# Kernel tuning notes

Measured on AMD Instinct MI355X. Metric: run time of the kernel, lower is better.

Reference implementation:

```python
import jax, jax.numpy as jnp
import numpy as np
from jax import lax

HEADS, DIM_HEAD, KSZ = 8, 64, 3


def conv1x1(x, w):
    # x: [B, Cin, X, Y], w: [Cout, Cin]
    return jnp.einsum('oi,bixy->boxy', w, x)


def setup_inputs() -> dict:
    key = jax.random.key(0)
    ks = jax.random.split(key, 8)
    dim = 256
    inner = HEADS * DIM_HEAD  # 512
    B, H, W = 4, 64, 64
    s = 0.02
    return {
        'fmap': jax.random.normal(ks[0], (B, dim, H, W), jnp.float32),
        'w_lin_q': jax.random.normal(ks[1], (inner, dim), jnp.float32) * s,
        'w_lin_kv_dw': jax.random.normal(ks[2], (dim, 1, 3, 3), jnp.float32) * s,
        'w_lin_kv_pw': jax.random.normal(ks[3], (2 * inner, dim), jnp.float32) * s,
        'w_q': jax.random.normal(ks[4], (inner, dim), jnp.float32) * s,
        'w_kv': jax.random.normal(ks[5], (2 * inner, dim), jnp.float32) * s,
        'w_out': jax.random.normal(ks[6], (dim, 2 * inner), jnp.float32) * s,
        'b_out': jax.random.normal(ks[7], (dim,), jnp.float32) * s,
    }


def reference(fmap, w_lin_q, w_lin_kv_dw, w_lin_kv_pw, w_q, w_kv, w_out, b_out):
    B, dim, X, Y = fmap.shape
    h, d, ksz = HEADS, DIM_HEAD, KSZ
    scale = d ** -0.5
    n = X * Y

    # ---- linear (global) attention branch ----
    # depthwise 3x3 conv (groups=dim) then pointwise 1x1, both bias-free
    dw = lax.conv_general_dilated(
        fmap, w_lin_kv_dw, window_strides=(1, 1), padding=[(1, 1), (1, 1)],
        dimension_numbers=('NCHW', 'OIHW', 'NCHW'), feature_group_count=dim)
    lin_kv = conv1x1(dw, w_lin_kv_pw)
    lin_q = conv1x1(fmap, w_lin_q)
    lin_k, lin_v = jnp.split(lin_kv, 2, axis=1)

    def to_bhnd(t):  # [B, h*d, X, Y] -> [B, h, n, d]
        return t.reshape(B, h, d, n).transpose(0, 1, 3, 2)

    lq, lk, lv = to_bhnd(lin_q), to_bhnd(lin_k), to_bhnd(lin_v)
    lq = jax.nn.softmax(lq, axis=-1) * scale   # softmax over feature dim
    lk = jax.nn.softmax(lk, axis=-2)           # softmax over sequence dim
    ctx = jnp.einsum('bhnd,bhne->bhde', lk, lv)
    lin_out = jnp.einsum('bhnd,bhde->bhne', lq, ctx)
    lin_out = lin_out.transpose(0, 1, 3, 2).reshape(B, h * d, X, Y)
    lin_out = jax.nn.gelu(lin_out, approximate=False)  # torch nn.GELU (exact erf)

    # ---- local window attention branch (unfold equivalent) ----
    q = conv1x1(fmap, w_q).reshape(B, h, d, X, Y) * scale
    kv = conv1x1(fmap, w_kv)
    k, v = jnp.split(kv, 2, axis=1)
    k = k.reshape(B, h, d, X, Y)
    v = v.reshape(B, h, d, X, Y)
    pad = ksz // 2
    padw = ((0, 0), (0, 0), (0, 0), (pad, pad), (pad, pad))
    kp = jnp.pad(k, padw)  # zero padding, as in F.unfold
    vp = jnp.pad(v, padw)
    # j enumerates kernel offsets row-major (ky, kx) -> matches F.unfold layout
    k_win = jnp.stack([kp[..., i:i + X, j:j + Y]
                       for i in range(ksz) for j in range(ksz)], axis=2)  # [B,h,j,d,X,Y]
    v_win = jnp.stack([vp[..., i:i + X, j:j + Y]
                       for i in range(ksz) for j in range(ksz)], axis=2)
    sim = jnp.einsum('bhdxy,bhjdxy->bhxyj', q, k_win)
    attn = jax.nn.softmax(sim, axis=-1)  # stable (max-subtracted internally)
    full = jnp.einsum('bhxyj,bhjdxy->bhdxy', attn, v_win)
    full = full.reshape(B, h * d, X, Y)

    out = jnp.concatenate([lin_out, full], axis=1)  # [B, 2*inner, X, Y]
    return conv1x1(out, w_out) + b_out[None, :, None, None]
```

## Files before the change

kernel.cpp:

```cpp
#include <hip/hip_runtime.h>
#include <cmath>

#define NPIX 4096
#define NTOT 16384
#define CIN  256

typedef __bf16 bf16x8 __attribute__((ext_vector_type(8)));
typedef float  f32x4  __attribute__((ext_vector_type(4)));
typedef unsigned short u16x8 __attribute__((ext_vector_type(8)));

static __device__ __forceinline__ unsigned short f2bf(float f) {
    unsigned u = __float_as_uint(f);
    unsigned r = (u + 0x7FFFu + ((u >> 16) & 1u)) >> 16;
    return (unsigned short)r;
}
static __device__ __forceinline__ float bf2f(unsigned short u) {
    return __uint_as_float((unsigned)u << 16);
}

__global__ __launch_bounds__(256) void k_transpose_bf(const float* __restrict__ src,
                                                      unsigned short* __restrict__ dst) {
    __shared__ float tile[64][65];
    int p0 = blockIdx.x * 64;
    int c0 = blockIdx.y * 64;
    int b  = blockIdx.z;
    int t = threadIdx.x;
    int tp = t & 63, tg = t >> 6;
    const float* s = src + ((size_t)(b * 256 + c0) * 4096) + p0;
#pragma unroll
    for (int r = 0; r < 16; ++r) {
        int c = r * 4 + tg;
        tile[tp][c] = s[(size_t)c * 4096 + tp];
    }
    __syncthreads();
    unsigned short* d = dst + ((size_t)(b * 4096 + p0)) * 256 + c0;
#pragma unroll
    for (int r = 0; r < 16; ++r) {
        int pr = r * 4 + tg;
        d[(size_t)pr * 256 + tp] = f2bf(tile[pr][tp]);
    }
}

__global__ __launch_bounds__(256) void k_dwconv_bf(const unsigned short* __restrict__ FMB,
                                                   const float* __restrict__ wdw,
                                                   unsigned short* __restrict__ DWB) {
    __shared__ float wl[2560];
    int t = threadIdx.x;
    for (int i = t; i < 2304; i += 256) wl[(i / 9) * 10 + (i % 9)] = wdw[i];
    __syncthreads();
    int idx = blockIdx.x * 256 + t;
    int cg = idx & 31, p = idx >> 5;
    int xy = p & 4095, x = xy >> 6, y = xy & 63;
    const unsigned short* base = FMB + (size_t)p * 256 + cg * 8;
    float s[8] = {0.f, 0.f, 0.f, 0.f, 0.f, 0.f, 0.f, 0.f};
#pragma unroll
    for (int dx = 0; dx < 3; ++dx) {
        int xx = x + dx - 1;
        if ((unsigned)xx >= 64u) continue;
#pragma unroll
        for (int dy = 0; dy < 3; ++dy) {
            int yy = y + dy - 1;
            if ((unsigned)yy >= 64u) continue;
            u16x8 v = *(const u16x8*)(base + ((dx - 1) * 64 + (dy - 1)) * 256);
#pragma unroll
            for (int d = 0; d < 8; ++d)
                s[d] += bf2f(v[d]) * wl[(cg * 8 + d) * 10 + dx * 3 + dy];
        }
    }
    uint4 w0;
    w0.x = (unsigned)f2bf(s[0]) | ((unsigned)f2bf(s[1]) << 16);
    w0.y = (unsigned)f2bf(s[2]) | ((unsigned)f2bf(s[3]) << 16);
    w0.z = (unsigned)f2bf(s[4]) | ((unsigned)f2bf(s[5]) << 16);
    w0.w = (unsigned)f2bf(s[6]) | ((unsigned)f2bf(s[7]) << 16);
    *(uint4*)(DWB + (size_t)p * 256 + cg * 8) = w0;
}

__global__ __launch_bounds__(256) void k_convert_w(const float* __restrict__ w1, const float* __restrict__ w2,
                                                   const float* __restrict__ w3, const float* __restrict__ w4,
                                                   const float* __restrict__ w5,
                                                   unsigned short* __restrict__ dst) {
    int i = blockIdx.x * 256 + threadIdx.x;
    float v;
    if (i < 131072)       v = w1[i];
    else if (i < 262144)  v = w2[i - 131072];
    else if (i < 524288)  v = w3[i - 262144];
    else if (i < 786432) {
        int elem = i - 524288;
        int rp = elem >> 8, c = elem & 255;
        int h = rp >> 7, wi = rp & 127;
        int srow = (wi < 64) ? (h * 64 + wi) : (512 + h * 64 + (wi - 64));
        v = w4[srow * 256 + c];
    } else                v = w5[i - 786432];
    dst[i] = f2bf(v);
}

__global__ __launch_bounds__(256) void k_qkv_gemm(const __bf16* __restrict__ FMB,
                                                  const __bf16* __restrict__ DWB,
                                                  const __bf16* __restrict__ WQKV,
                                                  const __bf16* __restrict__ WPW,
                                                  unsigned short* __restrict__ LQB,
                                                  unsigned short* __restrict__ CKV2,
                                                  float* __restrict__ PART,
                                                  float* __restrict__ S) {
    __shared__ __align__(16) __bf16 SMEM[128 * 136];
    __bf16* As = SMEM;
    __bf16* Bs = SMEM + 128 * 64;
    const int K = 256;
    const int m0 = blockIdx.x * 128;
    const int by = blockIdx.y;
    const bool g2 = (by >= 16);
    const __bf16* A = g2 ? DWB : FMB;
    const __bf16* B = g2 ? WPW : WQKV;
    const int n0 = (g2 ? by - 16 : by) * 128;
    const int t = threadIdx.x;
    const int w = t >> 6, l = t & 63;
    const int wm = (w >> 1) * 64, wn = (w & 1) * 64;
    f32x4 acc[4][4];
#pragma unroll
    for (int i = 0; i < 4; ++i)
#pragma unroll
        for (int j = 0; j < 4; ++j) acc[i][j] = (f32x4){0.f, 0.f, 0.f, 0.f};

    const int lrow = l >> 3;
    const int lchunk = (l & 7) ^ lrow;
    for (int k0 = 0; k0 < K; k0 += 64) {
#pragma unroll
        for (int r = 0; r < 4; ++r) {
            const int s = w + r * 4;
            const int row = s * 8 + lrow;
            const __bf16* ga = A + (size_t)(m0 + row) * K + (k0 + lchunk * 8);
            const __bf16* gb = B + (size_t)(n0 + row) * K + (k0 + lchunk * 8);
            __builtin_amdgcn_global_load_lds((const __attribute__((address_space(1))) void*)ga,
                                             (__attribute__((address_space(3))) void*)(As + s * 512),
                                             16, 0, 0);
            __builtin_amdgcn_global_load_lds((const __attribute__((address_space(1))) void*)gb,
                                             (__attribute__((address_space(3))) void*)(Bs + s * 512),
                                             16, 0, 0);
        }
        __syncthreads();
#pragma unroll
        for (int ks = 0; ks < 2; ++ks) {
            bf16x8 af[4], bfr[4];
#pragma unroll
            for (int i = 0; i < 4; ++i) {
                const int arow = wm + i * 16 + (l & 15);
                const int ac = ((l >> 4) + ks * 4) ^ (l & 7);
                af[i] = *(const bf16x8*)(As + arow * 64 + ac * 8);
                const int brow = wn + i * 16 + (l & 15);
                bfr[i] = *(const bf16x8*)(Bs + brow * 64 + ac * 8);
            }
#pragma unroll
            for (int i = 0; i < 4; ++i)
#pragma unroll
                for (int j = 0; j < 4; ++j)
                    acc[i][j] = __builtin_amdgcn_mfma_f32_16x16x32_bf16(af[i], bfr[j], acc[i][j], 0, 0, 0);
        }
        __syncthreads();
    }

    if (g2) {
        unsigned short* ST = (unsigned short*)SMEM;
#pragma unroll
        for (int i = 0; i < 4; ++i) {
            const int prow = wm + i * 16 + (l >> 4) * 4;
#pragma unroll
            for (int j = 0; j < 4; ++j) {
                const int col = wn + j * 16 + (l & 15);
#pragma unroll
                for (int q = 0; q < 4; ++q) {
                    float v = acc[i][j][q];
                    ST[col * 130 + prow + q] = f2bf(col < 64 ? __expf(v) : v);
                }
            }
        }
        __syncthreads();
        const int h  = n0 >> 7;
        const int bh = (m0 >> 12) * 8 + h;
        const int dm = (w >> 1) * 32, en = (w & 1) * 32;
        f32x4 c2[2][2];
        f32x4 s2[2];
#pragma unroll
        for (int i = 0; i < 2; ++i) {
            s2[i] = (f32x4){0.f, 0.f, 0.f, 0.f};
#pragma unroll
            for (int j = 0; j < 2; ++j) c2[i][j] = (f32x4){0.f, 0.f, 0.f, 0.f};
        }
        bf16x8 ones;
#pragma unroll
        for (int d = 0; d < 8; ++d) ones[d] = (__bf16)1.0f;
#pragma unroll
        for (int kp = 0; kp < 4; ++kp) {
            bf16x8 af2[2], bv2[2];
#pragma unroll
            for (int i = 0; i < 2; ++i) {
                const int drow = dm + i * 16 + (l & 15);
                af2[i] = *(const bf16x8*)(ST + drow * 130 + kp * 32 + (l >> 4) * 8);
                const int erow = 64 + en + i * 16 + (l & 15);
                bv2[i] = *(const bf16x8*)(ST + erow * 130 + kp * 32 + (l >> 4) * 8);
            }
#pragma unroll
            for (int i = 0; i < 2; ++i)
#pragma unroll
                for (int j = 0; j < 2; ++j)
                    c2[i][j] = __builtin_amdgcn_mfma_f32_16x16x32_bf16(af2[i], bv2[j], c2[i][j], 0, 0, 0);
            if ((w & 1) == 0)
#pragma unroll
                for (int i = 0; i < 2; ++i)
                    s2[i] = __builtin_amdgcn_mfma_f32_16x16x32_bf16(af2[i], ones, s2[i], 0, 0, 0);
        }
        float* pp = PART + ((size_t)((m0 >> 7) * 8 + h)) * 4096 + t * 16;
#pragma unroll
        for (int i = 0; i < 2; ++i)
#pragma unroll
            for (int j = 0; j < 2; ++j)
                *(f32x4*)(pp + (i * 2 + j) * 4) = c2[i][j];
        if ((w & 1) == 0 && (l & 15) == 0) {
#pragma unroll
            for (int i = 0; i < 2; ++i)
#pragma unroll
                for (int q = 0; q < 4; ++q)
                    atomicAdd(&S[bh * 64 + dm + i * 16 + (l >> 4) * 4 + q], s2[i][q]);
        }
        return;
    }

#pragma unroll
    for (int i = 0; i < 4; ++i) {
        const int prow = wm + i * 16 + (l >> 4) * 4;
#pragma unroll
        for (int j = 0; j < 4; ++j) {
            const int col = wn + j * 16 + (l & 15);
            const int cglob = n0 + col;
            const float sc = (cglob >= 512 && cglob < 1024) ? 0.125f : 1.f;
#pragma unroll
            for (int q = 0; q < 4; ++q)
                *((unsigned short*)SMEM + (prow + q) * 136 + col) = f2bf(acc[i][j][q] * sc);
        }
    }
    __syncthreads();
    const int pix = t >> 1, half = t & 1;
    const unsigned short* sp = (const unsigned short*)SMEM + pix * 136 + half * 64;
    if (n0 < 512) {
        float m = -1e30f;
#pragma unroll
        for (int r = 0; r < 8; ++r) {
            u16x8 v = *(const u16x8*)(sp + r * 8);
#pragma unroll
            for (int d = 0; d < 8; ++d) m = fmaxf(m, bf2f(v[d]));
        }
        float Z = 0.f;
#pragma unroll
        for (int r = 0; r < 8; ++r) {
            u16x8 v = *(const u16x8*)(sp + r * 8);
#pragma unroll
            for (int d = 0; d < 8; ++d) Z += __expf(bf2f(v[d]) - m);
        }
        float inv = 0.125f / Z;
        unsigned short* dst = LQB + (size_t)(m0 + pix) * 512 + n0 + half * 64;
#pragma unroll
        for (int r = 0; r < 8; ++r) {
            u16x8 v = *(const u16x8*)(sp + r * 8);
            float o[8];
#pragma unroll
            for (int d = 0; d < 8; ++d) o[d] = __expf(bf2f(v[d]) - m) * inv;
            uint4 wv;
            wv.x = (unsigned)f2bf(o[0]) | ((unsigned)f2bf(o[1]) << 16);
            wv.y = (unsigned)f2bf(o[2]) | ((unsigned)f2bf(o[3]) << 16);
            wv.z = (unsigned)f2bf(o[4]) | ((unsigned)f2bf(o[5]) << 16);
            wv.w = (unsigned)f2bf(o[6]) | ((unsigned)f2bf(o[7]) << 16);
            *(uint4*)(dst + r * 8) = wv;
        }
    } else {
        unsigned short* dptr = CKV2 + (size_t)(m0 + pix) * 1536 + (n0 - 512) + half * 64;
#pragma unroll
        for (int r = 0; r < 8; ++r)
            *(u16x8*)(dptr + r * 8) = *(const u16x8*)(sp + r * 8);
    }
}

__global__ __launch_bounds__(256) void k_ctxnorm(const float* __restrict__ PART,
                                                 const float* __restrict__ S,
                                                 unsigned short* __restrict__ ctxb) {
    __shared__ float SUM[1024];
    __shared__ float sinv[32];
    const int bh = blockIdx.x, wq = blockIdx.y;
    const int b = bh >> 3, h = bh & 7;
    const int t = threadIdx.x;
    const int bd = (wq >> 1) * 32, be = (wq & 1) * 32;
#pragma unroll
    for (int r = 0; r < 4; ++r) {
        const int kl = t + 256 * r;
        const float* src = PART + (size_t)((b * 32) * 8 + h) * 4096 + wq * 1024 + kl;
        float s = 0.f;
#pragma unroll
        for (int mi = 0; mi < 32; ++mi)
            s += src[(size_t)mi * 8 * 4096];
        SUM[kl] = s;
    }
    if (t < 32) sinv[t] = 1.f / S[bh * 64 + bd + t];
    __syncthreads();
#pragma unroll
    for (int r = 0; r < 4; ++r) {
        const int idx = t + 256 * r;
        const int dd = idx & 31, ee = idx >> 5;
        const int d = bd + dd, e = be + ee;
        const int l2 = (((d >> 2) & 3) << 4) | (e & 15);
        const int i2 = (d >> 4) & 1, j2 = (e >> 4) & 1, q = d & 3;
        const int kl = l2 * 16 + (i2 * 2 + j2) * 4 + q;
        ctxb[(size_t)bh * 4096 + e * 64 + d] = f2bf(SUM[kl] * sinv[dd]);
    }
}

__global__ __launch_bounds__(256) void k_out_gemm(const __bf16* __restrict__ A,
                                                  const __bf16* __restrict__ B,
                                                  float* __restrict__ C,
                                                  const float* __restrict__ bias) {
    __shared__ __align__(16) __bf16 SMEM[24576];
    const int K = 1024;
    const int m0 = blockIdx.x * 64, n0 = blockIdx.y * 128;
    const int t = threadIdx.x;
    const int w = t >> 6, l = t & 63;
    const int wm = (w >> 1) * 32, wn = (w & 1) * 64;
    f32x4 acc[2][4];
#pragma unroll
    for (int i = 0; i < 2; ++i)
#pragma unroll
        for (int j = 0; j < 4; ++j) acc[i][j] = (f32x4){0.f, 0.f, 0.f, 0.f};

    const int lrow = l >> 3;
    const int lchunk = (l & 7) ^ lrow;
    auto stage = [&](int buf, int k0) {
        __bf16* As = SMEM + buf * 12288;
        __bf16* Bs = As + 4096;
#pragma unroll
        for (int r = 0; r < 2; ++r) {
            const int s = w + r * 4;
            const int row = s * 8 + lrow;
            const __bf16* ga = A + (size_t)(m0 + row) * K + (k0 + lchunk * 8);
            __builtin_amdgcn_global_load_lds((const __attribute__((address_space(1))) void*)ga,
                                             (__attribute__((address_space(3))) void*)(As + s * 512),
                                             16, 0, 0);
        }
#pragma unroll
        for (int r = 0; r < 4; ++r) {
            const int s = w + r * 4;
            const int row = s * 8 + lrow;
            const __bf16* gb = B + (size_t)(n0 + row) * K + (k0 + lchunk * 8);
            __builtin_amdgcn_global_load_lds((const __attribute__((address_space(1))) void*)gb,
                                             (__attribute__((address_space(3))) void*)(Bs + s * 512),
                                             16, 0, 0);
        }
    };

    stage(0, 0);
    for (int it = 0; it < 16; ++it) {
        __syncthreads();
        if (it < 15) stage((it + 1) & 1, (it + 1) * 64);
        const __bf16* As = SMEM + (it & 1) * 12288;
        const __bf16* Bs = As + 4096;
#pragma unroll
        for (int ks = 0; ks < 2; ++ks) {
            const int ac = ((l >> 4) + ks * 4) ^ (l & 7);
            bf16x8 af[2], bfr[4];
#pragma unroll
            for (int i = 0; i < 2; ++i) {
                const int arow = wm + i * 16 + (l & 15);
                af[i] = *(const bf16x8*)(As + arow * 64 + ac * 8);
            }
#pragma unroll
            for (int j = 0; j < 4; ++j) {
                const int brow = wn + j * 16 + (l & 15);
                bfr[j] = *(const bf16x8*)(Bs + brow * 64 + ac * 8);
            }
#pragma unroll
            for (int i = 0; i < 2; ++i)
#pragma unroll
                for (int j = 0; j < 4; ++j)
                    acc[i][j] = __builtin_amdgcn_mfma_f32_16x16x32_bf16(af[i], bfr[j], acc[i][j], 0, 0, 0);
        }
    }
    const int b = m0 >> 12;
#pragma unroll
    for (int j = 0; j < 4; ++j) {
        const int col = n0 + wn + j * 16 + (l & 15);
        const float bv = bias[col];
        float* obase = C + ((size_t)(b * 256 + col) << 12);
#pragma unroll
        for (int i = 0; i < 2; ++i) {
            const int rb = (m0 & 4095) + wm + i * 16 + (l >> 4) * 4;
            f32x4 v = acc[i][j];
            v[0] += bv; v[1] += bv; v[2] += bv; v[3] += bv;
            *(f32x4*)(obase + rb) = v;
        }
    }
}

__global__ __launch_bounds__(256) void k_lin_mfma(const __bf16* __restrict__ LQB,
                                                  const __bf16* __restrict__ ctxb,
                                                  unsigned short* __restrict__ CAT) {
    const int p0 = blockIdx.x * 128;
    const int h  = blockIdx.y;
    const int b  = p0 >> 12;
    const int t = threadIdx.x, w = t >> 6, l = t & 63;
    const int wm = w * 32;
    const __bf16* Bm = ctxb + (size_t)(b * 8 + h) * 4096;
    f32x4 acc[2][4];
#pragma unroll
    for (int i = 0; i < 2; ++i)
#pragma unroll
        for (int j = 0; j < 4; ++j) acc[i][j] = (f32x4){0.f, 0.f, 0.f, 0.f};
#pragma unroll
    for (int ks = 0; ks < 2; ++ks) {
        const int c = (l >> 4) + ks * 4;
        bf16x8 af[2], bfr[4];
#pragma unroll
        for (int i = 0; i < 2; ++i) {
            const int row = p0 + wm + i * 16 + (l & 15);
            af[i] = *(const bf16x8*)(LQB + (size_t)row * 512 + h * 64 + c * 8);
        }
#pragma unroll
        for (int j = 0; j < 4; ++j) {
            const int erow = j * 16 + (l & 15);
            bfr[j] = *(const bf16x8*)(Bm + erow * 64 + c * 8);
        }
#pragma unroll
        for (int i = 0; i < 2; ++i)
#pragma unroll
            for (int j = 0; j < 4; ++j)
                acc[i][j] = __builtin_amdgcn_mfma_f32_16x16x32_bf16(af[i], bfr[j], acc[i][j], 0, 0, 0);
    }
#pragma unroll
    for (int i = 0; i < 2; ++i) {
#pragma unroll
        for (int j = 0; j < 4; ++j) {
            const int e = j * 16 + (l & 15);
#pragma unroll
            for (int q = 0; q < 4; ++q) {
                const int p = p0 + wm + i * 16 + (l >> 4) * 4 + q;
                float x = acc[i][j][q];
                float g = 0.5f * x * (1.f + erff(x * 0.70710678118654752f));
                CAT[(size_t)p * 1024 + h * 64 + e] = f2bf(g);
            }
        }
    }
}

__global__ __launch_bounds__(256) void k_local_attn(const unsigned short* __restrict__ CKV,
                                                    unsigned short* __restrict__ CAT) {
    const int W = blockIdx.x * 4 + (threadIdx.x >> 6);
    const int lane = threadIdx.x & 63;
    const int h = W & 7;
    const int G = W >> 3;
    const int yg = G & 7, x = (G >> 3) & 63, b = G >> 9;
    const int lg = lane >> 3, c8 = lane & 7;
    const int y = (yg << 3) + lg;
    const int p = (b << 12) + (x << 6) + y;
    const unsigned short* Qp = CKV + (size_t)p * 1536 + h * 64 + c8 * 8;
    const unsigned short* Kp = Qp + 512;
    const unsigned short* Vp = Qp + 1024;

    const bool okx[3] = {x > 0, true, x < 63};
    const bool oky[3] = {y > 0, true, y < 63};
    bool okn[9]; int ofs[9];
#pragma unroll
    for (int dx = 0; dx < 3; ++dx)
#pragma unroll
        for (int dy = 0; dy < 3; ++dy) {
            const int k = dx * 3 + dy;
            okn[k] = okx[dx] && oky[dy];
            ofs[k] = okn[k] ? ((dx - 1) * 64 + (dy - 1)) * 1536 : 0;
        }
    float qf[8];
    {
        u16x8 q8 = *(const u16x8*)Qp;
#pragma unroll
        for (int d = 0; d < 8; ++d) qf[d] = bf2f(q8[d]);
    }
    float sim[9];
#pragma unroll
    for (int k = 0; k < 9; ++k) {
        u16x8 k8 = *(const u16x8*)(Kp + ofs[k]);
        float s = 0.f;
#pragma unroll
        for (int d = 0; d < 8; ++d) s += qf[d] * bf2f(k8[d]);
        s = okn[k] ? s : 0.f;
        s += __shfl_xor(s, 1);
        s += __shfl_xor(s, 2);
        s += __shfl_xor(s, 4);
        sim[k] = s;
    }
    float mx = sim[0];
#pragma unroll
    for (int k = 1; k < 9; ++k) mx = fmaxf(mx, sim[k]);
    float a[9], Z = 0.f;
#pragma unroll
    for (int k = 0; k < 9; ++k) { a[k] = __expf(sim[k] - mx); Z += a[k]; }
    float inv = 1.f / Z;
#pragma unroll
    for (int k = 0; k < 9; ++k) a[k] = okn[k] ? a[k] * inv : 0.f;
    float o[8] = {0.f, 0.f, 0.f, 0.f, 0.f, 0.f, 0.f, 0.f};
#pragma unroll
    for (int k = 0; k < 9; ++k) {
        u16x8 v8 = *(const u16x8*)(Vp + ofs[k]);
#pragma unroll
        for (int d = 0; d < 8; ++d) o[d] += a[k] * bf2f(v8[d]);
    }
    unsigned short* dst = CAT + (size_t)p * 1024 + 512 + h * 64 + c8 * 8;
    uint4 w0;
    w0.x = (unsigned)f2bf(o[0]) | ((unsigned)f2bf(o[1]) << 16);
    w0.y = (unsigned)f2bf(o[2]) | ((unsigned)f2bf(o[3]) << 16);
    w0.z = (unsigned)f2bf(o[4]) | ((unsigned)f2bf(o[5]) << 16);
    w0.w = (unsigned)f2bf(o[6]) | ((unsigned)f2bf(o[7]) << 16);
    *(uint4*)dst = w0;
}

extern "C" void kernel_launch(void* const* d_in, const int* in_sizes, int n_in,
                              void* d_out, int out_size, void* d_ws, size_t ws_size,
                              hipStream_t stream) {
    const float* fmap  = (const float*)d_in[0];
    const float* w_lq  = (const float*)d_in[1];
    const float* w_dw  = (const float*)d_in[2];
    const float* w_pw  = (const float*)d_in[3];
    const float* w_q   = (const float*)d_in[4];
    const float* w_kv  = (const float*)d_in[5];
    const float* w_out = (const float*)d_in[6];
    const float* b_out = (const float*)d_in[7];
    float* out = (float*)d_out;

    unsigned short* base = (unsigned short*)d_ws;
    unsigned short* CATB = base;
    unsigned short* FMB  = base + (size_t)NTOT * 1024;
    unsigned short* DWB  = FMB + (size_t)NTOT * 256;
    unsigned short* WB   = DWB + (size_t)NTOT * 256;
    unsigned short* WQKV = WB;
    unsigned short* WPW  = WB + 524288;
    unsigned short* WOUT = WB + 786432;
    unsigned short* CTXB = WB + 1048576;
    unsigned short* LQB  = CTXB + 131072;
    unsigned short* CKV2 = LQB + (size_t)NTOT * 512;
    float* PART = (float*)(CKV2 + (size_t)NTOT * 1536);
    float* S    = PART + (size_t)1024 * 4096;

    k_transpose_bf<<<dim3(64, 4, 4), 256, 0, stream>>>(fmap, FMB);
    k_convert_w<<<4096, 256, 0, stream>>>(w_lq, w_q, w_kv, w_pw, w_out, WB);
    hipMemsetAsync(S, 0, 2048 * sizeof(float), stream);
    k_dwconv_bf<<<2048, 256, 0, stream>>>(FMB, w_dw, DWB);
    k_qkv_gemm<<<dim3(128, 24), 256, 0, stream>>>((const __bf16*)FMB, (const __bf16*)DWB,
                                                  (const __bf16*)WQKV, (const __bf16*)WPW,
                                                  LQB, CKV2, PART, S);
    k_ctxnorm<<<dim3(32, 4), 256, 0, stream>>>(PART, S, CTXB);
    k_lin_mfma<<<dim3(128, 8), 256, 0, stream>>>((const __bf16*)LQB, (const __bf16*)CTXB, CATB);
    k_local_attn<<<4096, 256, 0, stream>>>(CKV2, CATB);
    k_out_gemm<<<dim3(256, 2), 256, 0, stream>>>((const __bf16*)CATB, (const __bf16*)WOUT, out, b_out);
}
```

Before: 166.0 us.

## Double-buffer GEMM loads with prefetch depth two and merge lin/local attention kernels

The QKV GEMM now double-buffers its LDS tiles and issues the next two k-stages ahead, using explicit vmcnt waits and raw barriers in place of __syncthreads. The output GEMM likewise prefetches two stages ahead with partial vmcnt waits. The linear-attention MFMA kernel and the local window attention kernel are fused into one launch that branches on block index, which removes a launch and lets both workloads share the GPU. This adds more LDS per block in the QKV GEMM, which may lower occupancy, and relies on hand-counted vmcnt values being correct.

```diff
diff --git a/kernel.cpp b/kernel.cpp
--- a/kernel.cpp
+++ b/kernel.cpp
@@ -102,9 +102,7 @@
                                                   unsigned short* __restrict__ CKV2,
                                                   float* __restrict__ PART,
                                                   float* __restrict__ S) {
-    __shared__ __align__(16) __bf16 SMEM[128 * 136];
-    __bf16* As = SMEM;
-    __bf16* Bs = SMEM + 128 * 64;
+    __shared__ __align__(16) __bf16 SMEM[32768];
     const int K = 256;
     const int m0 = blockIdx.x * 128;
     const int by = blockIdx.y;
@@ -123,7 +121,7 @@
 
     const int lrow = l >> 3;
     const int lchunk = (l & 7) ^ lrow;
-    for (int k0 = 0; k0 < K; k0 += 64) {
+    auto STAGE = [&](int buf, int k0) {
 #pragma unroll
         for (int r = 0; r < 4; ++r) {
             const int s = w + r * 4;
@@ -131,13 +129,24 @@
             const __bf16* ga = A + (size_t)(m0 + row) * K + (k0 + lchunk * 8);
             const __bf16* gb = B + (size_t)(n0 + row) * K + (k0 + lchunk * 8);
             __builtin_amdgcn_global_load_lds((const __attribute__((address_space(1))) void*)ga,
-                                             (__attribute__((address_space(3))) void*)(As + s * 512),
+                                             (__attribute__((address_space(3))) void*)(SMEM + buf * 16384 + s * 512),
                                              16, 0, 0);
             __builtin_amdgcn_global_load_lds((const __attribute__((address_space(1))) void*)gb,
-                                             (__attribute__((address_space(3))) void*)(Bs + s * 512),
+                                             (__attribute__((address_space(3))) void*)(SMEM + buf * 16384 + 8192 + s * 512),
                                              16, 0, 0);
         }
-        __syncthreads();
+    };
+    STAGE(0, 0);
+    STAGE(1, 64);
+#pragma unroll
+    for (int it = 0; it < 4; ++it) {
+        if (it < 3) { asm volatile("s_waitcnt vmcnt(8)" ::: "memory"); }
+        else        { asm volatile("s_waitcnt vmcnt(0)" ::: "memory"); }
+        __builtin_amdgcn_sched_barrier(0);
+        __builtin_amdgcn_s_barrier();
+        __builtin_amdgcn_sched_barrier(0);
+        const __bf16* As = SMEM + (it & 1) * 16384;
+        const __bf16* Bs = As + 8192;
 #pragma unroll
         for (int ks = 0; ks < 2; ++ks) {
             bf16x8 af[4], bfr[4];
@@ -155,7 +164,10 @@
                 for (int j = 0; j < 4; ++j)
                     acc[i][j] = __builtin_amdgcn_mfma_f32_16x16x32_bf16(af[i], bfr[j], acc[i][j], 0, 0, 0);
         }
-        __syncthreads();
+        __builtin_amdgcn_sched_barrier(0);
+        __builtin_amdgcn_s_barrier();
+        __builtin_amdgcn_sched_barrier(0);
+        if (it < 2) STAGE(it & 1, (it + 2) * 64);
     }
 
     if (g2) {
@@ -329,7 +341,7 @@
 
     const int lrow = l >> 3;
     const int lchunk = (l & 7) ^ lrow;
-    auto stage = [&](int buf, int k0) {
+    auto STAGE = [&](int buf, int k0) {
         __bf16* As = SMEM + buf * 12288;
         __bf16* Bs = As + 4096;
 #pragma unroll
@@ -352,10 +364,14 @@
         }
     };
 
-    stage(0, 0);
+    STAGE(0, 0);
+    STAGE(1, 64);
     for (int it = 0; it < 16; ++it) {
-        __syncthreads();
-        if (it < 15) stage((it + 1) & 1, (it + 1) * 64);
+        if (it < 15) { asm volatile("s_waitcnt vmcnt(6)" ::: "memory"); }
+        else         { asm volatile("s_waitcnt vmcnt(0)" ::: "memory"); }
+        __builtin_amdgcn_sched_barrier(0);
+        __builtin_amdgcn_s_barrier();
+        __builtin_amdgcn_sched_barrier(0);
         const __bf16* As = SMEM + (it & 1) * 12288;
         const __bf16* Bs = As + 4096;
 #pragma unroll
@@ -378,6 +394,10 @@
                 for (int j = 0; j < 4; ++j)
                     acc[i][j] = __builtin_amdgcn_mfma_f32_16x16x32_bf16(af[i], bfr[j], acc[i][j], 0, 0, 0);
         }
+        __builtin_amdgcn_sched_barrier(0);
+        __builtin_amdgcn_s_barrier();
+        __builtin_amdgcn_sched_barrier(0);
+        if (it < 14) STAGE(it & 1, (it + 2) * 64);
     }
     const int b = m0 >> 12;
 #pragma unroll
@@ -395,123 +415,125 @@
     }
 }
 
-__global__ __launch_bounds__(256) void k_lin_mfma(const __bf16* __restrict__ LQB,
+__global__ __launch_bounds__(256) void k_linlocal(const __bf16* __restrict__ LQB,
                                                   const __bf16* __restrict__ ctxb,
+                                                  const unsigned short* __restrict__ CKV,
                                                   unsigned short* __restrict__ CAT) {
-    const int p0 = blockIdx.x * 128;
-    const int h  = blockIdx.y;
-    const int b  = p0 >> 12;
-    const int t = threadIdx.x, w = t >> 6, l = t & 63;
-    const int wm = w * 32;
-    const __bf16* Bm = ctxb + (size_t)(b * 8 + h) * 4096;
-    f32x4 acc[2][4];
-#pragma unroll
-    for (int i = 0; i < 2; ++i)
-#pragma unroll
-        for (int j = 0; j < 4; ++j) acc[i][j] = (f32x4){0.f, 0.f, 0.f, 0.f};
-#pragma unroll
-    for (int ks = 0; ks < 2; ++ks) {
-        const int c = (l >> 4) + ks * 4;
-        bf16x8 af[2], bfr[4];
+    const int bid = blockIdx.x;
+    const int t = threadIdx.x;
+    if (bid < 1024) {
+        const int p0 = (bid & 127) * 128;
+        const int h  = bid >> 7;
+        const int b  = p0 >> 12;
+        const int w = t >> 6, l = t & 63;
+        const int wm = w * 32;
+        const __bf16* Bm = ctxb + (size_t)(b * 8 + h) * 4096;
+        f32x4 acc[2][4];
+#pragma unroll
+        for (int i = 0; i < 2; ++i)
+#pragma unroll
+            for (int j = 0; j < 4; ++j) acc[i][j] = (f32x4){0.f, 0.f, 0.f, 0.f};
+#pragma unroll
+        for (int ks = 0; ks < 2; ++ks) {
+            const int c = (l >> 4) + ks * 4;
+            bf16x8 af[2], bfr[4];
+#pragma unroll
+            for (int i = 0; i < 2; ++i) {
+                const int row = p0 + wm + i * 16 + (l & 15);
+                af[i] = *(const bf16x8*)(LQB + (size_t)row * 512 + h * 64 + c * 8);
+            }
+#pragma unroll
+            for (int j = 0; j < 4; ++j) {
+                const int erow = j * 16 + (l & 15);
+                bfr[j] = *(const bf16x8*)(Bm + erow * 64 + c * 8);
+            }
+#pragma unroll
+            for (int i = 0; i < 2; ++i)
+#pragma unroll
+                for (int j = 0; j < 4; ++j)
+                    acc[i][j] = __builtin_amdgcn_mfma_f32_16x16x32_bf16(af[i], bfr[j], acc[i][j], 0, 0, 0);
+        }
 #pragma unroll
         for (int i = 0; i < 2; ++i) {
-            const int row = p0 + wm + i * 16 + (l & 15);
-            af[i] = *(const bf16x8*)(LQB + (size_t)row * 512 + h * 64 + c * 8);
-        }
-#pragma unroll
-        for (int j = 0; j < 4; ++j) {
-            const int erow = j * 16 + (l & 15);
-            bfr[j] = *(const bf16x8*)(Bm + erow * 64 + c * 8);
-        }
-#pragma unroll
-        for (int i = 0; i < 2; ++i)
-#pragma unroll
-            for (int j = 0; j < 4; ++j)
-                acc[i][j] = __builtin_amdgcn_mfma_f32_16x16x32_bf16(af[i], bfr[j], acc[i][j], 0, 0, 0);
-    }
-#pragma unroll
-    for (int i = 0; i < 2; ++i) {
-#pragma unroll
-        for (int j = 0; j < 4; ++j) {
-            const int e = j * 16 + (l & 15);
-#pragma unroll
-            for (int q = 0; q < 4; ++q) {
-                const int p = p0 + wm + i * 16 + (l >> 4) * 4 + q;
-                float x = acc[i][j][q];
-                float g = 0.5f * x * (1.f + erff(x * 0.70710678118654752f));
-                CAT[(size_t)p * 1024 + h * 64 + e] = f2bf(g);
-            }
-        }
-    }
-}
-
-__global__ __launch_bounds__(256) void k_local_attn(const unsigned short* __restrict__ CKV,
-                                                    unsigned short* __restrict__ CAT) {
-    const int W = blockIdx.x * 4 + (threadIdx.x >> 6);
-    const int lane = threadIdx.x & 63;
-    const int h = W & 7;
-    const int G = W >> 3;
-    const int yg = G & 7, x = (G >> 3) & 63, b = G >> 9;
-    const int lg = lane >> 3, c8 = lane & 7;
-    const int y = (yg << 3) + lg;
-    const int p = (b << 12) + (x << 6) + y;
-    const unsigned short* Qp = CKV + (size_t)p * 1536 + h * 64 + c8 * 8;
-    const unsigned short* Kp = Qp + 512;
-    const unsigned short* Vp = Qp + 1024;
-
-    const bool okx[3] = {x > 0, true, x < 63};
-    const bool oky[3] = {y > 0, true, y < 63};
-    bool okn[9]; int ofs[9];
-#pragma unroll
-    for (int dx = 0; dx < 3; ++dx)
-#pragma unroll
-        for (int dy = 0; dy < 3; ++dy) {
-            const int k = dx * 3 + dy;
-            okn[k] = okx[dx] && oky[dy];
-            ofs[k] = okn[k] ? ((dx - 1) * 64 + (dy - 1)) * 1536 : 0;
-        }
-    float qf[8];
-    {
-        u16x8 q8 = *(const u16x8*)Qp;
-#pragma unroll
-        for (int d = 0; d < 8; ++d) qf[d] = bf2f(q8[d]);
-    }
-    float sim[9];
-#pragma unroll
-    for (int k = 0; k < 9; ++k) {
-        u16x8 k8 = *(const u16x8*)(Kp + ofs[k]);
-        float s = 0.f;
-#pragma unroll
-        for (int d = 0; d < 8; ++d) s += qf[d] * bf2f(k8[d]);
-        s = okn[k] ? s : 0.f;
-        s += __shfl_xor(s, 1);
-        s += __shfl_xor(s, 2);
-        s += __shfl_xor(s, 4);
-        sim[k] = s;
-    }
-    float mx = sim[0];
-#pragma unroll
-    for (int k = 1; k < 9; ++k) mx = fmaxf(mx, sim[k]);
-    float a[9], Z = 0.f;
-#pragma unroll
-    for (int k = 0; k < 9; ++k) { a[k] = __expf(sim[k] - mx); Z += a[k]; }
-    float inv = 1.f / Z;
-#pragma unroll
-    for (int k = 0; k < 9; ++k) a[k] = okn[k] ? a[k] * inv : 0.f;
-    float o[8] = {0.f, 0.f, 0.f, 0.f, 0.f, 0.f, 0.f, 0.f};
-#pragma unroll
-    for (int k = 0; k < 9; ++k) {
-        u16x8 v8 = *(const u16x8*)(Vp + ofs[k]);
-#pragma unroll
-        for (int d = 0; d < 8; ++d) o[d] += a[k] * bf2f(v8[d]);
-    }
-    unsigned short* dst = CAT + (size_t)p * 1024 + 512 + h * 64 + c8 * 8;
-    uint4 w0;
-    w0.x = (unsigned)f2bf(o[0]) | ((unsigned)f2bf(o[1]) << 16);
-    w0.y = (unsigned)f2bf(o[2]) | ((unsigned)f2bf(o[3]) << 16);
-    w0.z = (unsigned)f2bf(o[4]) | ((unsigned)f2bf(o[5]) << 16);
-    w0.w = (unsigned)f2bf(o[6]) | ((unsigned)f2bf(o[7]) << 16);
-    *(uint4*)dst = w0;
+#pragma unroll
+            for (int j = 0; j < 4; ++j) {
+                const int e = j * 16 + (l & 15);
+#pragma unroll
+                for (int q = 0; q < 4; ++q) {
+                    const int p = p0 + wm + i * 16 + (l >> 4) * 4 + q;
+                    float x = acc[i][j][q];
+                    float g = 0.5f * x * (1.f + erff(x * 0.70710678118654752f));
+                    CAT[(size_t)p * 1024 + h * 64 + e] = f2bf(g);
+                }
+            }
+        }
+    } else {
+        const int W = (bid - 1024) * 4 + (t >> 6);
+        const int lane = t & 63;
+        const int h = W & 7;
+        const int G = W >> 3;
+        const int yg = G & 7, x = (G >> 3) & 63, b = G >> 9;
+        const int lg = lane >> 3, c8 = lane & 7;
+        const int y = (yg << 3) + lg;
+        const int p = (b << 12) + (x << 6) + y;
+        const unsigned short* Qp = CKV + (size_t)p * 1536 + h * 64 + c8 * 8;
+        const unsigned short* Kp = Qp + 512;
+        const unsigned short* Vp = Qp + 1024;
+
+        const bool okx[3] = {x > 0, true, x < 63};
+        const bool oky[3] = {y > 0, true, y < 63};
+        bool okn[9]; int ofs[9];
+#pragma unroll
+        for (int dx = 0; dx < 3; ++dx)
+#pragma unroll
+            for (int dy = 0; dy < 3; ++dy) {
+                const int k = dx * 3 + dy;
+                okn[k] = okx[dx] && oky[dy];
+                ofs[k] = okn[k] ? ((dx - 1) * 64 + (dy - 1)) * 1536 : 0;
+            }
+        float qf[8];
+        {
+            u16x8 q8 = *(const u16x8*)Qp;
+#pragma unroll
+            for (int d = 0; d < 8; ++d) qf[d] = bf2f(q8[d]);
+        }
+        float sim[9];
+#pragma unroll
+        for (int k = 0; k < 9; ++k) {
+            u16x8 k8 = *(const u16x8*)(Kp + ofs[k]);
+            float s = 0.f;
+#pragma unroll
+            for (int d = 0; d < 8; ++d) s += qf[d] * bf2f(k8[d]);
+            s = okn[k] ? s : 0.f;
+            s += __shfl_xor(s, 1);
+            s += __shfl_xor(s, 2);
+            s += __shfl_xor(s, 4);
+            sim[k] = s;
+        }
+        float mx = sim[0];
+#pragma unroll
+        for (int k = 1; k < 9; ++k) mx = fmaxf(mx, sim[k]);
+        float a[9], Z = 0.f;
+#pragma unroll
+        for (int k = 0; k < 9; ++k) { a[k] = __expf(sim[k] - mx); Z += a[k]; }
+        float inv = 1.f / Z;
+#pragma unroll
+        for (int k = 0; k < 9; ++k) a[k] = okn[k] ? a[k] * inv : 0.f;
+        float o[8] = {0.f, 0.f, 0.f, 0.f, 0.f, 0.f, 0.f, 0.f};
+#pragma unroll
+        for (int k = 0; k < 9; ++k) {
+            u16x8 v8 = *(const u16x8*)(Vp + ofs[k]);
+#pragma unroll
+            for (int d = 0; d < 8; ++d) o[d] += a[k] * bf2f(v8[d]);
+        }
+        unsigned short* dst = CAT + (size_t)p * 1024 + 512 + h * 64 + c8 * 8;
+        uint4 w0;
+        w0.x = (unsigned)f2bf(o[0]) | ((unsigned)f2bf(o[1]) << 16);
+        w0.y = (unsigned)f2bf(o[2]) | ((unsigned)f2bf(o[3]) << 16);
+        w0.z = (unsigned)f2bf(o[4]) | ((unsigned)f2bf(o[5]) << 16);
+        w0.w = (unsigned)f2bf(o[6]) | ((unsigned)f2bf(o[7]) << 16);
+        *(uint4*)dst = w0;
+    }
 }
 
 extern "C" void kernel_launch(void* const* d_in, const int* in_sizes, int n_in,
@@ -549,7 +571,6 @@
                                                   (const __bf16*)WQKV, (const __bf16*)WPW,
                                                   LQB, CKV2, PART, S);
     k_ctxnorm<<<dim3(32, 4), 256, 0, stream>>>(PART, S, CTXB);
-    k_lin_mfma<<<dim3(128, 8), 256, 0, stream>>>((const __bf16*)LQB, (const __bf16*)CTXB, CATB);
-    k_local_attn<<<4096, 256, 0, stream>>>(CKV2, CATB);
+    k_linlocal<<<5120, 256, 0, stream>>>((const __bf16*)LQB, (const __bf16*)CTXB, CKV2, CATB);
     k_out_gemm<<<dim3(256, 2), 256, 0, stream>>>((const __bf16*)CATB, (const __bf16*)WOUT, out, b_out);
 }
```

After: 161.8 us. 1.03x faster.
